# Kernel tuning notes

Measured on AMD Instinct MI355X. Metric: run time of the kernel, lower is better.

Reference implementation:

```python
import jax, jax.numpy as jnp
import numpy as np

N = 50_000          # nodes
E = 1_600_000       # edges (avg degree 32)
IN = 128            # in_feats
H = 4               # num_heads
F = 32              # out_feats per head
CUTOFF = 4.0        # bessel_cutoff
P = 7               # envelope_exponent + 1
ENV_A = -(P + 1) * (P + 2) / 2.0   # -36
ENV_B = P * (P + 2)                # 63
ENV_C = -P * (P + 1) / 2.0         # -28


def setup_inputs() -> dict:
    key = jax.random.key(0)
    ks = jax.random.split(key, 8)
    x = jax.random.normal(ks[0], (N, IN), dtype=jnp.float32)
    distance = jax.random.uniform(ks[1], (E,), dtype=jnp.float32) * CUTOFF
    W_src = jax.random.normal(ks[2], (H * F, IN), dtype=jnp.float32) * 0.05
    b_src = jnp.zeros((H * F,), dtype=jnp.float32)
    W_dst = jax.random.normal(ks[3], (H * F, IN), dtype=jnp.float32) * 0.05
    b_dst = jnp.zeros((H * F,), dtype=jnp.float32)
    attn = jax.random.normal(ks[4], (1, H, F), dtype=jnp.float32) * 0.1
    prelu_alpha = jnp.full((H,), 0.25, dtype=jnp.float32)
    frequencies = jnp.arange(1.0, H + 1.0, dtype=jnp.float32) * np.pi
    src = jax.random.randint(ks[5], (E,), 0, N, dtype=jnp.int32)
    dst = jax.random.randint(ks[6], (E,), 0, N, dtype=jnp.int32)
    return dict(x=x, distance=distance, W_src=W_src, b_src=b_src,
                W_dst=W_dst, b_dst=b_dst, attn=attn,
                prelu_alpha=prelu_alpha, frequencies=frequencies,
                src=src, dst=dst)


def _bessel_coeff(distance, frequencies):
    # distance: [E] -> d_scaled: [E,1]; frequencies: [H] -> coeff: [E,H]
    d = (distance / CUTOFF)[:, None]
    d_p0 = d ** P
    env = d + ENV_A * d_p0 + ENV_B * (d_p0 * d) + ENV_C * (d_p0 * d * d)
    return env * jnp.sin(frequencies * d)


def reference(x, distance, W_src, b_src, W_dst, b_dst, attn,
              prelu_alpha, frequencies, src, dst):
    n = x.shape[0]
    feat_src = (x @ W_src.T + b_src).reshape(n, H, F)   # [N,H,F]
    feat_dst = (x @ W_dst.T + b_dst).reshape(n, H, F)   # [N,H,F]

    coeff = _bessel_coeff(distance, frequencies)[:, :, None]  # [E,H,1]

    el = feat_src[src]                                  # [E,H,F] gather
    e = (el + feat_dst[dst]) * coeff                    # u_add_v then bessel scale
    e = jnp.where(e >= 0, e, prelu_alpha[None, :, None] * e)  # PReLU per head
    score = jnp.einsum('ehf,hf->eh', e, attn[0])        # [E,H]

    # edge softmax over incoming edges per dst node, per head
    seg_max = jax.ops.segment_max(score, dst, num_segments=n)        # [N,H]
    ex = jnp.exp(score - seg_max[dst])                               # [E,H]
    denom = jax.ops.segment_sum(ex, dst, num_segments=n)             # [N,H]
    a = ex / denom[dst]                                              # [E,H]

    # u_mul_e + scatter-sum aggregation
    msgs = el * a[:, :, None]                                        # [E,H,F]
    rst = jax.ops.segment_sum(msgs, dst, num_segments=n)             # [N,H,F]
    return rst
```

## Files before the change

kernel.cpp:

```cpp
#include <hip/hip_runtime.h>
#include <hip/hip_bf16.h>
#include <math.h>

#define N_NODES 50000
#define E_EDGES 1600000
#define HF 128
#define INV_CUTOFF 0.25f
#define ENV_A -36.0f
#define ENV_B 63.0f
#define ENV_C -28.0f

#define GEMM_BLOCKS ((N_NODES + 63) / 64)
#define REC_CAP 72
#define NBUCK 196
#define BUCK_CAP 8960
#define EPB 6250
#define SPLIT 4
#define LCAP 32

typedef __attribute__((ext_vector_type(8))) short bf16x8;
typedef __attribute__((ext_vector_type(4))) float f32x4;

__device__ __forceinline__ unsigned short f2bf(float f) {
  unsigned u = __float_as_uint(f);
  u += 0x7fffu + ((u >> 16) & 1u);
  return (unsigned short)(u >> 16);
}
__device__ __forceinline__ unsigned pack2(float lo, float hi) {
  return (unsigned)f2bf(lo) | ((unsigned)f2bf(hi) << 16);
}
__device__ __forceinline__ float2 up2(unsigned v) {
  return make_float2(__uint_as_float(v << 16), __uint_as_float(v & 0xffff0000u));
}

__device__ __forceinline__ float2 pk_add(float2 a, float2 b) {
  float2 d;
  asm("v_pk_add_f32 %0, %1, %2" : "=v"(d) : "v"(a), "v"(b));
  return d;
}
__device__ __forceinline__ float2 pk_fma(float2 a, float2 b, float2 c) {
  float2 d;
  asm("v_pk_fma_f32 %0, %1, %2, %3" : "=v"(d) : "v"(a), "v"(b), "v"(c));
  return d;
}
__device__ __forceinline__ float2 pk_abs(float2 a) {
  float2 d;
  d.x = __uint_as_float(__float_as_uint(a.x) & 0x7fffffffu);
  d.y = __uint_as_float(__float_as_uint(a.y) & 0x7fffffffu);
  return d;
}

__global__ void prep_w(const float* __restrict__ Ws, const float* __restrict__ Wd,
                       unsigned short* __restrict__ wbf) {
  const int q = blockIdx.x * 256 + threadIdx.x;
  if (q < 4096) {
    const int n = q >> 4, c = q & 15;
    const float* Wp = ((n < 128) ? Ws : Wd) + (size_t)(n & 127) * HF + c * 8;
    const float4 v0 = *(const float4*)Wp;
    const float4 v1 = *(const float4*)(Wp + 4);
    uint4 pk;
    pk.x = pack2(v0.x, v0.y); pk.y = pack2(v0.z, v0.w);
    pk.z = pack2(v1.x, v1.y); pk.w = pack2(v1.z, v1.w);
    *(uint4*)(wbf + (size_t)n * HF + ((c ^ (n & 15)) * 8)) = pk;
  }
}

__global__ __launch_bounds__(256) void feat_gemm(
    const float* __restrict__ x, const unsigned short* __restrict__ wbf,
    const float* __restrict__ bs, const float* __restrict__ bd,
    unsigned short* __restrict__ fs, float* __restrict__ fd) {
  __shared__ unsigned short wlds[256 * 128];

  for (int i = threadIdx.x; i < 4096; i += 256)
    ((uint4*)wlds)[i] = ((const uint4*)wbf)[i];

  const int lane = threadIdx.x & 63;
  const int wave = threadIdx.x >> 6;
  const int m = lane & 15;
  const int quad = lane >> 4;
  const int m0 = blockIdx.x * 64 + wave * 16;
  const int row = m0 + m;
  const int rowc = (row < N_NODES) ? row : (N_NODES - 1);

  union { bf16x8 v; unsigned u[4]; } af[4];
  #pragma unroll
  for (int kt = 0; kt < 4; kt++) {
    const float* xp = x + (size_t)rowc * HF + kt * 32 + quad * 8;
    const float4 u0 = *(const float4*)xp;
    const float4 u1 = *(const float4*)(xp + 4);
    af[kt].u[0] = pack2(u0.x, u0.y); af[kt].u[1] = pack2(u0.z, u0.w);
    af[kt].u[2] = pack2(u1.x, u1.y); af[kt].u[3] = pack2(u1.z, u1.w);
  }

  __syncthreads();

  float accA[16][4];
  #pragma unroll
  for (int nt = 0; nt < 16; nt++) {
    const int nrow = nt * 16 + m;
    f32x4 acc = {0.f, 0.f, 0.f, 0.f};
    #pragma unroll
    for (int kt = 0; kt < 4; kt++) {
      const int pc = (kt * 4 + quad) ^ m;
      const bf16x8 bf = *(const bf16x8*)(wlds + (size_t)nrow * HF + pc * 8);
      acc = __builtin_amdgcn_mfma_f32_16x16x32_bf16(af[kt].v, bf, acc, 0, 0, 0);
    }
    accA[nt][0] = acc[0]; accA[nt][1] = acc[1];
    accA[nt][2] = acc[2]; accA[nt][3] = acc[3];
  }

  __syncthreads();
  unsigned short* fsS = wlds;
  float* fdS = (float*)(wlds + 64 * 136);

  const int rl0 = wave * 16 + quad * 4;
  #pragma unroll
  for (int nt = 0; nt < 16; nt++) {
    const int col = nt * 16 + m;
    if (col < 128) {
      const float bias = bs[col];
      #pragma unroll
      for (int r = 0; r < 4; r++)
        fsS[(rl0 + r) * 136 + col] = f2bf(accA[nt][r] + bias);
    } else {
      const float bias = bd[col - 128];
      #pragma unroll
      for (int r = 0; r < 4; r++)
        fdS[(rl0 + r) * 132 + (col - 128)] = accA[nt][r] + bias;
    }
  }
  __syncthreads();

  for (int c = threadIdx.x; c < 1024; c += 256) {
    const int r = c >> 4, off = (c & 15) * 8;
    const int gr = blockIdx.x * 64 + r;
    if (gr < N_NODES)
      *(uint4*)(fs + (size_t)gr * HF + off) = *(const uint4*)(fsS + r * 136 + off);
  }
  for (int c = threadIdx.x; c < 2048; c += 256) {
    const int r = c >> 5, off = (c & 31) * 4;
    const int gr = blockIdx.x * 64 + r;
    if (gr < N_NODES)
      *(float4*)(fd + (size_t)gr * HF + off) = *(const float4*)(fdS + r * 132 + off);
  }
}

__global__ __launch_bounds__(256) void bucketize(
    const int* __restrict__ dst, const int* __restrict__ src,
    const float* __restrict__ dist,
    int* __restrict__ bcursor, unsigned* __restrict__ bb_pay,
    unsigned char* __restrict__ bb_loc) {
  __shared__ unsigned pay_s[EPB];
  __shared__ unsigned char bkt_s[EPB];
  __shared__ unsigned char loc_s[EPB];
  __shared__ int hist[NBUCK], loff[NBUCK], base[NBUCK], cur[NBUCK];
  for (int t = threadIdx.x; t < NBUCK; t += 256) { hist[t] = 0; cur[t] = 0; }
  __syncthreads();
  const int lo = blockIdx.x * EPB;
  for (int k = threadIdx.x; k < EPB; k += 256)
    atomicAdd(&hist[dst[lo + k] >> 8], 1);
  __syncthreads();
  if (threadIdx.x == 0) {
    int run = 0;
    for (int j = 0; j < NBUCK; j++) { loff[j] = run; run += hist[j]; }
  }
  __syncthreads();
  for (int t = threadIdx.x; t < NBUCK; t += 256)
    base[t] = atomicAdd(&bcursor[t], hist[t]);
  __syncthreads();
  for (int k = threadIdx.x; k < EPB; k += 256) {
    const int d = dst[lo + k];
    const int b = d >> 8;
    float ds = dist[lo + k] * (INV_CUTOFF * 65536.f);
    unsigned dq = (unsigned)(ds + 0.5f);
    if (dq > 65535u) dq = 65535u;
    const int s = loff[b] + atomicAdd(&cur[b], 1);
    pay_s[s] = (unsigned)src[lo + k] | (dq << 16);
    bkt_s[s] = (unsigned char)b;
    loc_s[s] = (unsigned char)(d & 255);
  }
  __syncthreads();
  for (int s = threadIdx.x; s < EPB; s += 256) {
    const int b = bkt_s[s];
    const int dest = base[b] + (s - loff[b]);
    if (dest < BUCK_CAP) {
      bb_pay[(size_t)b * BUCK_CAP + dest] = pay_s[s];
      bb_loc[(size_t)b * BUCK_CAP + dest] = loc_s[s];
    }
  }
}

__global__ __launch_bounds__(256) void bucket_scatter(
    const int* __restrict__ bcursor, const unsigned* __restrict__ bb_pay,
    const unsigned char* __restrict__ bb_loc,
    int* __restrict__ counts, unsigned* __restrict__ rec) {
  __shared__ int cnt[256];
  __shared__ unsigned recS[256 * LCAP];
  cnt[threadIdx.x] = 0;
  __syncthreads();
  const int b = blockIdx.x / SPLIT;
  const int q = blockIdx.x - b * SPLIT;
  const int total = min(bcursor[b], BUCK_CAP);
  const int lo = (total * q) / SPLIT;
  const int hi = (total * (q + 1)) / SPLIT;
  const size_t base = (size_t)b * BUCK_CAP;
  for (int i = lo + threadIdx.x; i < hi; i += 256) {
    const unsigned pay = bb_pay[base + i];
    const int local = bb_loc[base + i];
    const int r = atomicAdd(&cnt[local], 1);
    if (r < LCAP) recS[local * LCAP + r] = pay;
  }
  __syncthreads();
  const int node = (b << 8) + (int)threadIdx.x;
  if (node < N_NODES) {
    const int cl = min(cnt[threadIdx.x], LCAP);
    if (cl > 0) {
      const int gbase = atomicAdd(&counts[node], cl);
      unsigned* dstp = rec + (size_t)node * REC_CAP;
      const unsigned* srcp = recS + threadIdx.x * LCAP;
      for (int k = 0; k < cl; k++) {
        const int pos = gbase + k;
        if (pos < REC_CAP) dstp[pos] = srcp[k];
      }
    }
  }
}

__global__ __launch_bounds__(256) void gat_agg(
    const unsigned short* __restrict__ fs, const float* __restrict__ fd,
    const int* __restrict__ counts, const unsigned* __restrict__ rec,
    const float* __restrict__ attn, const float* __restrict__ alpha_p,
    const float* __restrict__ freqs, float* __restrict__ out) {
  const int wave = threadIdx.x >> 6;
  const int lane = threadIdx.x & 63;
  const int node = blockIdx.x * 4 + wave;
  if (node >= N_NODES) return;
  const int eslot = lane >> 4;
  const int h = (lane >> 2) & 3;
  const int j = lane & 3;
  const int fo = (h << 5) + (j << 3);

  int cnt = counts[node];
  cnt = (cnt < REC_CAP) ? cnt : REC_CAP;

  if (cnt <= 0) {
    if (eslot == 0) {
      float* o = out + (size_t)node * HF + fo;
      float4 z = {0.f, 0.f, 0.f, 0.f};
      *(float4*)o = z;
      *(float4*)(o + 4) = z;
    }
    return;
  }

  const float* fdp = fd + (size_t)node * HF + fo;
  const float2 f0 = *(const float2*)(fdp + 0);
  const float2 f1 = *(const float2*)(fdp + 2);
  const float2 f2 = *(const float2*)(fdp + 4);
  const float2 f3 = *(const float2*)(fdp + 6);
  const float2 t0 = *(const float2*)(attn + fo + 0);
  const float2 t1 = *(const float2*)(attn + fo + 2);
  const float2 t2 = *(const float2*)(attn + fo + 4);
  const float2 t3 = *(const float2*)(attn + fo + 6);
  const float al = alpha_p[h];
  const float c1 = 0.5f * (1.0f + al);
  const float c2 = 0.5f * (1.0f - al);
  const float fr = freqs[h];

  const int beg = node * REC_CAP;
  const int end = beg + cnt;
  const int last = end - 1;
  const unsigned short* fsp = fs + fo;

  int e0i = beg + eslot;
  unsigned rcur = rec[(e0i < end) ? e0i : last];
  uint4 ebcur = *(const uint4*)(fsp + ((size_t)(rcur & 0xffffu) << 7));
  int e1i = beg + 4 + eslot;
  unsigned rnext = rec[(e1i < end) ? e1i : last];

  float l = 0.f;
  float2 A0 = {0.f, 0.f}, A1 = {0.f, 0.f}, A2 = {0.f, 0.f}, A3 = {0.f, 0.f};

  for (int i = beg; i < end; i += 4) {
    const unsigned r = rcur;
    const uint4 eb = ebcur;
    rcur = rnext;
    const int inn = i + 8 + eslot;
    rnext = rec[(inn < end) ? inn : last];
    ebcur = *(const uint4*)(fsp + ((size_t)(rcur & 0xffffu) << 7));

    const bool valid = (i + eslot < end);
    const float d = (float)(r >> 16) * (1.0f / 65536.0f);
    const float2 e0 = up2(eb.x);
    const float2 e1 = up2(eb.y);
    const float2 e2 = up2(eb.z);
    const float2 e3 = up2(eb.w);

    const float d2 = d * d;
    const float d4 = d2 * d2;
    const float d7 = d4 * d2 * d;
    const float env = fmaf(d7, fmaf(d, fmaf(d, ENV_C, ENV_B), ENV_A), d);
    const float cf = env * __sinf(fr * d);
    const float k1 = c1 * cf;
    const float k2 = c2 * fabsf(cf);

    float2 D1 = {0.f, 0.f}, D2 = {0.f, 0.f};
    float2 u;
    u = pk_add(e0, f0); D1 = pk_fma(u, t0, D1); D2 = pk_fma(pk_abs(u), t0, D2);
    u = pk_add(e1, f1); D1 = pk_fma(u, t1, D1); D2 = pk_fma(pk_abs(u), t1, D2);
    u = pk_add(e2, f2); D1 = pk_fma(u, t2, D1); D2 = pk_fma(pk_abs(u), t2, D2);
    u = pk_add(e3, f3); D1 = pk_fma(u, t3, D1); D2 = pk_fma(pk_abs(u), t3, D2);

    float p = fmaf(k1, D1.x + D1.y, k2 * (D2.x + D2.y));
    p += __shfl_xor(p, 1);
    p += __shfl_xor(p, 2);

    const float w = valid ? __expf(p) : 0.f;
    l += w;
    const float2 w2 = {w, w};
    A0 = pk_fma(w2, e0, A0);
    A1 = pk_fma(w2, e1, A1);
    A2 = pk_fma(w2, e2, A2);
    A3 = pk_fma(w2, e3, A3);
  }

  #pragma unroll
  for (int mm = 16; mm < 64; mm <<= 1) {
    l    += __shfl_xor(l, mm);
    A0.x += __shfl_xor(A0.x, mm); A0.y += __shfl_xor(A0.y, mm);
    A1.x += __shfl_xor(A1.x, mm); A1.y += __shfl_xor(A1.y, mm);
    A2.x += __shfl_xor(A2.x, mm); A2.y += __shfl_xor(A2.y, mm);
    A3.x += __shfl_xor(A3.x, mm); A3.y += __shfl_xor(A3.y, mm);
  }

  if (eslot == 0) {
    const float rl = (l > 0.f) ? 1.0f / l : 0.f;
    float* o = out + (size_t)node * HF + fo;
    float4 o0 = {A0.x * rl, A0.y * rl, A1.x * rl, A1.y * rl};
    float4 o1 = {A2.x * rl, A2.y * rl, A3.x * rl, A3.y * rl};
    *(float4*)o = o0;
    *(float4*)(o + 4) = o1;
  }
}

extern "C" void kernel_launch(void* const* d_in, const int* in_sizes, int n_in,
                              void* d_out, int out_size, void* d_ws, size_t ws_size,
                              hipStream_t stream) {
  const float* x      = (const float*)d_in[0];
  const float* dist   = (const float*)d_in[1];
  const float* W_src  = (const float*)d_in[2];
  const float* b_src  = (const float*)d_in[3];
  const float* W_dst  = (const float*)d_in[4];
  const float* b_dst  = (const float*)d_in[5];
  const float* attn   = (const float*)d_in[6];
  const float* alpha  = (const float*)d_in[7];
  const float* freqs  = (const float*)d_in[8];
  const int*   src    = (const int*)d_in[9];
  const int*   dst    = (const int*)d_in[10];
  float* out = (float*)d_out;

  char* w = (char*)d_ws;
  size_t off = 0;
  auto alloc = [&](size_t bytes) -> void* {
    void* p = w + off;
    off += (bytes + 255) & ~(size_t)255;
    return p;
  };
  unsigned short* feat_src = (unsigned short*)alloc((size_t)N_NODES * HF * 2);
  float*          feat_dst = (float*)alloc((size_t)N_NODES * HF * 4);
  unsigned short* wbf      = (unsigned short*)alloc((size_t)256 * HF * 2);
  int*            counts   = (int*)alloc((size_t)N_NODES * 4);
  int*            bcursor  = (int*)alloc((size_t)NBUCK * 4);
  unsigned*       bb_pay   = (unsigned*)alloc((size_t)NBUCK * BUCK_CAP * 4);
  unsigned char*  bb_loc   = (unsigned char*)alloc((size_t)NBUCK * BUCK_CAP);
  unsigned*       rec      = (unsigned*)alloc((size_t)NBUCK * 256 * REC_CAP * 4);

  hipMemsetAsync(bcursor, 0, (size_t)NBUCK * 4, stream);
  hipMemsetAsync(counts, 0, (size_t)N_NODES * 4, stream);

  prep_w<<<16, 256, 0, stream>>>(W_src, W_dst, wbf);

  feat_gemm<<<GEMM_BLOCKS, 256, 0, stream>>>(x, wbf, b_src, b_dst, feat_src, feat_dst);

  bucketize<<<256, 256, 0, stream>>>(dst, src, dist, bcursor, bb_pay, bb_loc);

  bucket_scatter<<<NBUCK * SPLIT, 256, 0, stream>>>(bcursor, bb_pay, bb_loc, counts, rec);

  gat_agg<<<(N_NODES + 3) / 4, 256, 0, stream>>>(
      feat_src, feat_dst, counts, rec, attn, alpha, freqs, out);
}
```

Baseline: 253.0 us.

## Process two nodes per wave in GAT aggregation with 16-feature lanes

New measurement: 248.8 us. Within noise of the previous version (-1.7%).

```diff
diff --git a/kernel.cpp b/kernel.cpp
--- a/kernel.cpp
+++ b/kernel.cpp
@@ -233,69 +233,51 @@
     const float* __restrict__ freqs, float* __restrict__ out) {
   const int wave = threadIdx.x >> 6;
   const int lane = threadIdx.x & 63;
-  const int node = blockIdx.x * 4 + wave;
-  if (node >= N_NODES) return;
-  const int eslot = lane >> 4;
-  const int h = (lane >> 2) & 3;
-  const int j = lane & 3;
-  const int fo = (h << 5) + (j << 3);
-
-  int cnt = counts[node];
+  const int n = lane >> 5;
+  const int e = (lane >> 3) & 3;
+  const int h = (lane >> 1) & 3;
+  const int j = lane & 1;
+  const int fo = (h << 5) + (j << 4);
+
+  const int node = blockIdx.x * 8 + wave * 2 + n;
+  const bool vnode = (node < N_NODES);
+  const int nodec = vnode ? node : (N_NODES - 1);
+
+  int cnt = vnode ? counts[node] : 0;
   cnt = (cnt < REC_CAP) ? cnt : REC_CAP;
 
-  if (cnt <= 0) {
-    if (eslot == 0) {
-      float* o = out + (size_t)node * HF + fo;
-      float4 z = {0.f, 0.f, 0.f, 0.f};
-      *(float4*)o = z;
-      *(float4*)(o + 4) = z;
-    }
-    return;
-  }
-
-  const float* fdp = fd + (size_t)node * HF + fo;
-  const float2 f0 = *(const float2*)(fdp + 0);
-  const float2 f1 = *(const float2*)(fdp + 2);
-  const float2 f2 = *(const float2*)(fdp + 4);
-  const float2 f3 = *(const float2*)(fdp + 6);
-  const float2 t0 = *(const float2*)(attn + fo + 0);
-  const float2 t1 = *(const float2*)(attn + fo + 2);
-  const float2 t2 = *(const float2*)(attn + fo + 4);
-  const float2 t3 = *(const float2*)(attn + fo + 6);
+  const float* fdp = fd + (size_t)nodec * HF + fo;
+  float2 f0 = *(const float2*)(fdp + 0),  f1 = *(const float2*)(fdp + 2);
+  float2 f2 = *(const float2*)(fdp + 4),  f3 = *(const float2*)(fdp + 6);
+  float2 f4 = *(const float2*)(fdp + 8),  f5 = *(const float2*)(fdp + 10);
+  float2 f6 = *(const float2*)(fdp + 12), f7 = *(const float2*)(fdp + 14);
+  const float* tp = attn + fo;
+  float2 t0 = *(const float2*)(tp + 0),  t1 = *(const float2*)(tp + 2);
+  float2 t2 = *(const float2*)(tp + 4),  t3 = *(const float2*)(tp + 6);
+  float2 t4 = *(const float2*)(tp + 8),  t5 = *(const float2*)(tp + 10);
+  float2 t6 = *(const float2*)(tp + 12), t7 = *(const float2*)(tp + 14);
+
   const float al = alpha_p[h];
   const float c1 = 0.5f * (1.0f + al);
   const float c2 = 0.5f * (1.0f - al);
   const float fr = freqs[h];
 
-  const int beg = node * REC_CAP;
-  const int end = beg + cnt;
-  const int last = end - 1;
+  const int beg = nodec * REC_CAP;
   const unsigned short* fsp = fs + fo;
 
-  int e0i = beg + eslot;
-  unsigned rcur = rec[(e0i < end) ? e0i : last];
-  uint4 ebcur = *(const uint4*)(fsp + ((size_t)(rcur & 0xffffu) << 7));
-  int e1i = beg + 4 + eslot;
-  unsigned rnext = rec[(e1i < end) ? e1i : last];
-
   float l = 0.f;
-  float2 A0 = {0.f, 0.f}, A1 = {0.f, 0.f}, A2 = {0.f, 0.f}, A3 = {0.f, 0.f};
-
-  for (int i = beg; i < end; i += 4) {
-    const unsigned r = rcur;
-    const uint4 eb = ebcur;
-    rcur = rnext;
-    const int inn = i + 8 + eslot;
-    rnext = rec[(inn < end) ? inn : last];
-    ebcur = *(const uint4*)(fsp + ((size_t)(rcur & 0xffffu) << 7));
-
-    const bool valid = (i + eslot < end);
+  float2 A0 = {0.f,0.f}, A1 = {0.f,0.f}, A2 = {0.f,0.f}, A3 = {0.f,0.f};
+  float2 A4 = {0.f,0.f}, A5 = {0.f,0.f}, A6 = {0.f,0.f}, A7 = {0.f,0.f};
+
+  for (int idx = e; idx < cnt; idx += 4) {
+    const unsigned r = rec[beg + idx];
+    const unsigned short* rowp = fsp + ((size_t)(r & 0xffffu) << 7);
+    const uint4 b0 = *(const uint4*)(rowp);
+    const uint4 b1 = *(const uint4*)(rowp + 8);
+    const float2 e0 = up2(b0.x), e1 = up2(b0.y), e2 = up2(b0.z), e3 = up2(b0.w);
+    const float2 e4 = up2(b1.x), e5 = up2(b1.y), e6 = up2(b1.z), e7 = up2(b1.w);
+
     const float d = (float)(r >> 16) * (1.0f / 65536.0f);
-    const float2 e0 = up2(eb.x);
-    const float2 e1 = up2(eb.y);
-    const float2 e2 = up2(eb.z);
-    const float2 e3 = up2(eb.w);
-
     const float d2 = d * d;
     const float d4 = d2 * d2;
     const float d7 = d4 * d2 * d;
@@ -310,36 +292,47 @@
     u = pk_add(e1, f1); D1 = pk_fma(u, t1, D1); D2 = pk_fma(pk_abs(u), t1, D2);
     u = pk_add(e2, f2); D1 = pk_fma(u, t2, D1); D2 = pk_fma(pk_abs(u), t2, D2);
     u = pk_add(e3, f3); D1 = pk_fma(u, t3, D1); D2 = pk_fma(pk_abs(u), t3, D2);
+    u = pk_add(e4, f4); D1 = pk_fma(u, t4, D1); D2 = pk_fma(pk_abs(u), t4, D2);
+    u = pk_add(e5, f5); D1 = pk_fma(u, t5, D1); D2 = pk_fma(pk_abs(u), t5, D2);
+    u = pk_add(e6, f6); D1 = pk_fma(u, t6, D1); D2 = pk_fma(pk_abs(u), t6, D2);
+    u = pk_add(e7, f7); D1 = pk_fma(u, t7, D1); D2 = pk_fma(pk_abs(u), t7, D2);
 
     float p = fmaf(k1, D1.x + D1.y, k2 * (D2.x + D2.y));
     p += __shfl_xor(p, 1);
-    p += __shfl_xor(p, 2);
-
-    const float w = valid ? __expf(p) : 0.f;
+
+    const float w = __expf(p);
     l += w;
     const float2 w2 = {w, w};
-    A0 = pk_fma(w2, e0, A0);
-    A1 = pk_fma(w2, e1, A1);
-    A2 = pk_fma(w2, e2, A2);
-    A3 = pk_fma(w2, e3, A3);
+    A0 = pk_fma(w2, e0, A0); A1 = pk_fma(w2, e1, A1);
+    A2 = pk_fma(w2, e2, A2); A3 = pk_fma(w2, e3, A3);
+    A4 = pk_fma(w2, e4, A4); A5 = pk_fma(w2, e5, A5);
+    A6 = pk_fma(w2, e6, A6); A7 = pk_fma(w2, e7, A7);
   }
 
   #pragma unroll
-  for (int mm = 16; mm < 64; mm <<= 1) {
+  for (int mm = 8; mm <= 16; mm <<= 1) {
     l    += __shfl_xor(l, mm);
     A0.x += __shfl_xor(A0.x, mm); A0.y += __shfl_xor(A0.y, mm);
     A1.x += __shfl_xor(A1.x, mm); A1.y += __shfl_xor(A1.y, mm);
     A2.x += __shfl_xor(A2.x, mm); A2.y += __shfl_xor(A2.y, mm);
     A3.x += __shfl_xor(A3.x, mm); A3.y += __shfl_xor(A3.y, mm);
-  }
-
-  if (eslot == 0) {
+    A4.x += __shfl_xor(A4.x, mm); A4.y += __shfl_xor(A4.y, mm);
+    A5.x += __shfl_xor(A5.x, mm); A5.y += __shfl_xor(A5.y, mm);
+    A6.x += __shfl_xor(A6.x, mm); A6.y += __shfl_xor(A6.y, mm);
+    A7.x += __shfl_xor(A7.x, mm); A7.y += __shfl_xor(A7.y, mm);
+  }
+
+  if (e == 0 && vnode) {
     const float rl = (l > 0.f) ? 1.0f / l : 0.f;
     float* o = out + (size_t)node * HF + fo;
     float4 o0 = {A0.x * rl, A0.y * rl, A1.x * rl, A1.y * rl};
     float4 o1 = {A2.x * rl, A2.y * rl, A3.x * rl, A3.y * rl};
-    *(float4*)o = o0;
-    *(float4*)(o + 4) = o1;
+    float4 o2 = {A4.x * rl, A4.y * rl, A5.x * rl, A5.y * rl};
+    float4 o3 = {A6.x * rl, A6.y * rl, A7.x * rl, A7.y * rl};
+    *(float4*)(o + 0)  = o0;
+    *(float4*)(o + 4)  = o1;
+    *(float4*)(o + 8)  = o2;
+    *(float4*)(o + 12) = o3;
   }
 }
 
@@ -386,6 +379,6 @@
 
   bucket_scatter<<<NBUCK * SPLIT, 256, 0, stream>>>(bcursor, bb_pay, bb_loc, counts, rec);
 
-  gat_agg<<<(N_NODES + 3) / 4, 256, 0, stream>>>(
+  gat_agg<<<(N_NODES + 7) / 8, 256, 0, stream>>>(
       feat_src, feat_dst, counts, rec, attn, alpha, freqs, out);
 }
```
